# Optimization experiments

Hardware: AMD Instinct MI355X
Metric: run time of the kernel (lower is better)

## Reference

```python
import jax, jax.numpy as jnp
import numpy as np

DIM = 1024
SEQ = 32768
BATCH = 1
MIN_ACTIVE = 0.01
MAX_ACTIVE = 0.1
KMAX = int(MAX_ACTIVE * DIM) + 1  # static upper bound on dynamic k (<= 102)
EPS = 1e-6


def setup_inputs() -> dict:
    key = jax.random.key(0)
    ks = jax.random.split(key, 7)
    h = DIM // 8
    s = 0.02
    return {
        "x": jax.random.normal(ks[0], (BATCH, SEQ, DIM), jnp.float32),
        # complexity_net: Linear(dim, dim//8) -> GELU -> Linear(dim//8, 1) -> Sigmoid
        "w1": jax.random.normal(ks[1], (DIM, h), jnp.float32) * s,
        "b1": jnp.zeros((h,), jnp.float32),
        "w2": jax.random.normal(ks[2], (h, 1), jnp.float32) * s,
        "b2": jnp.zeros((1,), jnp.float32),
        # gate_net: Linear(dim, dim)
        "wg": jax.random.normal(ks[3], (DIM, DIM), jnp.float32) * s,
        "bg": jnp.zeros((DIM,), jnp.float32),
        # running stats (eval mode: used for normalization, not updated)
        "running_mean": jax.random.normal(ks[4], (DIM,), jnp.float32) * 0.1,
        "running_var": jax.random.uniform(ks[5], (DIM,), jnp.float32, minval=0.5, maxval=1.5),
    }


def reference(x, w1, b1, w2, b2, wg, bg, running_mean, running_var):
    # complexity from seq-mean pooled features -> scalar in (0,1)
    pooled = x.mean(axis=1, keepdims=True)                      # (B,1,D)
    hid = jax.nn.gelu(pooled @ w1 + b1, approximate=False)      # torch GELU is exact erf
    complexity = jax.nn.sigmoid(hid @ w2 + b2)                  # (B,1,1)
    active_ratio = MIN_ACTIVE + (MAX_ACTIVE - MIN_ACTIVE) * complexity
    # torch .int() truncates; clamp(min=1). B==1 so k is effectively scalar.
    k = jnp.clip((active_ratio * DIM).astype(jnp.int32), 1, KMAX)  # (B,1,1)

    importance = jnp.abs(x @ wg + bg)                           # (B,S,D)
    importance = (importance - running_mean) / (jnp.sqrt(running_var) + EPS)

    # dynamic-k topk via static-KMAX top_k + threshold at the k-th largest value
    topk_vals, _ = jax.lax.top_k(importance, KMAX)              # (B,S,KMAX)
    idx = jnp.broadcast_to((k - 1).astype(jnp.int32), (x.shape[0], x.shape[1], 1))
    kth = jnp.take_along_axis(topk_vals, idx, axis=-1)          # (B,S,1)
    mask = (importance >= kth).astype(x.dtype)                  # (B,S,D), non-differentiable
    mask = jax.lax.stop_gradient(mask)

    # straight-through combine: forward = x*mask, backward passes grad to all of x
    sparse_x = x * mask + (x - jax.lax.stop_gradient(x)) * (1.0 - mask)

    complexity_mean = complexity.mean()
    active_ratio_mean = active_ratio.mean()
    active_neurons = k.astype(jnp.float32).mean()
    return sparse_x, complexity_mean, active_ratio_mean, active_neurons
```

## Files before the change

kernel.cpp:

```cpp
#include <hip/hip_runtime.h>
#include <cstdint>
#include <cstddef>

#define SEQ 32768
#define DIM 1024
#define HID 128
#define KMAXV 103

using f4 = __attribute__((ext_vector_type(4))) float;
using f2 = __attribute__((ext_vector_type(2))) float;

__global__ __launch_bounds__(256) void pool_partial(const float* __restrict__ x,
                                                    double* __restrict__ part) {
    const int b = blockIdx.x;
    const int t = threadIdx.x;
    const int r0 = b * 128;
    double s0 = 0.0, s1 = 0.0, s2 = 0.0, s3 = 0.0;
    for (int r = 0; r < 128; ++r) {
        const float* row = x + (size_t)(r0 + r) * DIM;
        s0 += (double)row[t];
        s1 += (double)row[t + 256];
        s2 += (double)row[t + 512];
        s3 += (double)row[t + 768];
    }
    double* p = part + (size_t)b * DIM;
    p[t] = s0; p[t + 256] = s1; p[t + 512] = s2; p[t + 768] = s3;
}

__global__ __launch_bounds__(1024) void tiny_net(const double* __restrict__ part,
                                                 const float* __restrict__ w1,
                                                 const float* __restrict__ b1,
                                                 const float* __restrict__ w2,
                                                 const float* __restrict__ b2,
                                                 float* __restrict__ out_scalars,
                                                 int* __restrict__ kout) {
    __shared__ double pooled[DIM];
    __shared__ double hidv[HID];
    const int t = threadIdx.x;

    double s = 0.0;
    for (int b = 0; b < 256; ++b) s += part[(size_t)b * DIM + t];
    pooled[t] = s / (double)SEQ;
    __syncthreads();

    if (t < HID) {
        double h = (double)b1[t];
        for (int d = 0; d < DIM; ++d) h += pooled[d] * (double)w1[d * HID + t];
        h = 0.5 * h * (1.0 + erf(h * 0.70710678118654752440));
        hidv[t] = h;
    }
    __syncthreads();

    if (t == 0) {
        double z = (double)b2[0];
        for (int j = 0; j < HID; ++j) z += hidv[j] * (double)w2[j];
        double c = 1.0 / (1.0 + exp(-z));
        double ar = 0.01 + 0.09 * c;
        int k = (int)(ar * (double)DIM);
        if (k < 1) k = 1;
        if (k > KMAXV) k = KMAXV;
        out_scalars[0] = (float)c;
        out_scalars[1] = (float)ar;
        out_scalars[2] = (float)k;
        *kout = k;
    }
}

#define BM 16
#define CBLOCK 512

template<int K0, int K1, int MODE>
__global__ __launch_bounds__(CBLOCK) void panel_kernel(const float* __restrict__ x,
                                                       const float* __restrict__ wg,
                                                       const float* __restrict__ bg,
                                                       const float* __restrict__ rm,
                                                       const float* __restrict__ rv,
                                                       const int* __restrict__ kptr,
                                                       float* __restrict__ out) {
    __shared__ float lbuf[(MODE == 2) ? 8 * DIM : 1];

    const int t = threadIdx.x;
    const int c2 = t << 1;
    const int row0 = blockIdx.x * BM;

    float pacc[16][2];
#pragma unroll
    for (int m = 0; m < 16; ++m) { pacc[m][0] = 0.0f; pacc[m][1] = 0.0f; }

    const float* wbase = wg + c2;

    f2 wc0 = *(const f2*)(wbase + (size_t)(K0 + 0) * DIM);
    f2 wc1 = *(const f2*)(wbase + (size_t)(K0 + 1) * DIM);
    f2 wc2 = *(const f2*)(wbase + (size_t)(K0 + 2) * DIM);
    f2 wc3 = *(const f2*)(wbase + (size_t)(K0 + 3) * DIM);

    for (int kk0 = K0; kk0 < K1; kk0 += 4) {
        const int kn = (kk0 + 4 < K1) ? (kk0 + 4) : K0;
        const f2 wn0 = *(const f2*)(wbase + (size_t)(kn + 0) * DIM);
        const f2 wn1 = *(const f2*)(wbase + (size_t)(kn + 1) * DIM);
        const f2 wn2 = *(const f2*)(wbase + (size_t)(kn + 2) * DIM);
        const f2 wn3 = *(const f2*)(wbase + (size_t)(kn + 3) * DIM);

        const float* xp = x + (size_t)row0 * DIM + kk0;
#pragma unroll
        for (int m = 0; m < 16; ++m) {
            const f4 xq = *(const f4*)(xp + m * DIM);
            float a0 = pacc[m][0], a1 = pacc[m][1];
            a0 = fmaf(xq[0], wc0[0], a0); a1 = fmaf(xq[0], wc0[1], a1);
            a0 = fmaf(xq[1], wc1[0], a0); a1 = fmaf(xq[1], wc1[1], a1);
            a0 = fmaf(xq[2], wc2[0], a0); a1 = fmaf(xq[2], wc2[1], a1);
            a0 = fmaf(xq[3], wc3[0], a0); a1 = fmaf(xq[3], wc3[1], a1);
            pacc[m][0] = a0; pacc[m][1] = a1;
        }
        wc0 = wn0; wc1 = wn1; wc2 = wn2; wc3 = wn3;
    }

    if constexpr (MODE == 0) {
#pragma unroll
        for (int m = 0; m < 16; ++m) {
            f2 v; v[0] = pacc[m][0]; v[1] = pacc[m][1];
            *(f2*)(out + (size_t)(row0 + m) * DIM + c2) = v;
        }
        return;
    } else if constexpr (MODE == 1) {
#pragma unroll
        for (int m = 0; m < 16; ++m) {
            float* op = out + (size_t)(row0 + m) * DIM + c2;
            f2 d = *(const f2*)op;
            d[0] = d[0] + pacc[m][0];
            d[1] = d[1] + pacc[m][1];
            *(f2*)op = d;
        }
        return;
    } else {
        float dot[16][2];
#pragma unroll
        for (int m = 0; m < 16; ++m) {
            const f2 d = *(const f2*)(out + (size_t)(row0 + m) * DIM + c2);
            dot[m][0] = d[0] + pacc[m][0];
            dot[m][1] = d[1] + pacc[m][1];
        }

        const f2 vbg = *(const f2*)(bg + c2);
        const f2 vrm = *(const f2*)(rm + c2);
        const f2 vrv = *(const f2*)(rv + c2);
        f2 vden;
        vden[0] = sqrtf(vrv[0]) + 1e-6f;
        vden[1] = sqrtf(vrv[1]) + 1e-6f;

        f2 imp[16];
#pragma unroll
        for (int m = 0; m < 16; ++m) {
            imp[m][0] = (fabsf(dot[m][0] + vbg[0]) - vrm[0]) / vden[0];
            imp[m][1] = (fabsf(dot[m][1] + vbg[1]) - vrm[1]) / vden[1];
        }

        int kval = *kptr;
        if (kval < 1) kval = 1;
        if (kval > DIM) kval = DIM;

        float (*selbuf)[DIM] = (float (*)[DIM])lbuf;

        for (int ch = 0; ch < 2; ++ch) {
            __syncthreads();
#pragma unroll
            for (int m = 0; m < 8; ++m)
                *(f2*)(&selbuf[m][c2]) = imp[ch * 8 + m];
            __syncthreads();

            const int w = t >> 6;
            const int l = t & 63;
            const size_t srow = (size_t)(row0 + ch * 8 + w);

            unsigned keys[16];
#pragma unroll
            for (int j = 0; j < 4; ++j) {
                const f4 v = *(const f4*)(&selbuf[w][4 * l + 256 * j]);
#pragma unroll
                for (int i = 0; i < 4; ++i) {
                    const unsigned u = __float_as_uint(v[i]);
                    keys[j * 4 + i] = (u & 0x80000000u) ? ~u : (u | 0x80000000u);
                }
            }

            unsigned pref = 0u;
            for (int b = 31; b >= 0; --b) {
                const unsigned tt = pref | (1u << b);
                int cnt = 0;
#pragma unroll
                for (int j = 0; j < 16; ++j) cnt += (keys[j] >= tt) ? 1 : 0;
#pragma unroll
                for (int off = 32; off >= 1; off >>= 1) cnt += __shfl_xor(cnt, off, 64);
                if (cnt >= kval) pref = tt;
            }

            const float* xr = x + srow * DIM;
            float* orow = out + srow * DIM;
#pragma unroll
            for (int j = 0; j < 4; ++j) {
                const f4 xv = *(const f4*)(xr + 4 * l + 256 * j);
                f4 o;
#pragma unroll
                for (int i = 0; i < 4; ++i) o[i] = (keys[j * 4 + i] >= pref) ? xv[i] : 0.0f;
                *(f4*)(orow + 4 * l + 256 * j) = o;
            }
        }
    }
}

extern "C" void kernel_launch(void* const* d_in, const int* in_sizes, int n_in,
                              void* d_out, int out_size, void* d_ws, size_t ws_size,
                              hipStream_t stream) {
    const float* x  = (const float*)d_in[0];
    const float* w1 = (const float*)d_in[1];
    const float* b1 = (const float*)d_in[2];
    const float* w2 = (const float*)d_in[3];
    const float* b2 = (const float*)d_in[4];
    const float* wg = (const float*)d_in[5];
    const float* bg = (const float*)d_in[6];
    const float* rm = (const float*)d_in[7];
    const float* rv = (const float*)d_in[8];
    float* out = (float*)d_out;

    double* part = (double*)d_ws;
    int* kptr = (int*)((char*)d_ws + (size_t)256 * DIM * sizeof(double));

    pool_partial<<<256, 256, 0, stream>>>(x, part);
    tiny_net<<<1, 1024, 0, stream>>>(part, w1, b1, w2, b2,
                                     out + (size_t)SEQ * DIM, kptr);
    panel_kernel<0,   384,  0><<<SEQ / BM, CBLOCK, 0, stream>>>(x, wg, bg, rm, rv, kptr, out);
    panel_kernel<384, 704,  1><<<SEQ / BM, CBLOCK, 0, stream>>>(x, wg, bg, rm, rv, kptr, out);
    panel_kernel<704, 1024, 2><<<SEQ / BM, CBLOCK, 0, stream>>>(x, wg, bg, rm, rv, kptr, out);
}
```

Baseline: 1.059 ms.

## Fuse second and third K-panels into one kernel and deepen weight prefetch

Merges the second and third K-range panel launches into a single kernel that holds the partial dot products in registers between them. This removes one launch and one full write and read-back of the partial sums through global memory. The weight prefetch is also deepened from one to two stages of four rows. The price is more live registers, which could lower occupancy or cause spills given the already large per-thread accumulator arrays.

Measured after the change: 1.045 ms. Within noise of the previous version (-1.3%).

```diff
diff --git a/kernel.cpp b/kernel.cpp
--- a/kernel.cpp
+++ b/kernel.cpp
@@ -69,37 +69,29 @@
 #define BM 16
 #define CBLOCK 512
 
-template<int K0, int K1, int MODE>
-__global__ __launch_bounds__(CBLOCK) void panel_kernel(const float* __restrict__ x,
-                                                       const float* __restrict__ wg,
-                                                       const float* __restrict__ bg,
-                                                       const float* __restrict__ rm,
-                                                       const float* __restrict__ rv,
-                                                       const int* __restrict__ kptr,
-                                                       float* __restrict__ out) {
-    __shared__ float lbuf[(MODE == 2) ? 8 * DIM : 1];
-
-    const int t = threadIdx.x;
-    const int c2 = t << 1;
-    const int row0 = blockIdx.x * BM;
-
-    float pacc[16][2];
+template<int K0, int K1>
+__device__ __forceinline__ void panel_acc(const float* __restrict__ x,
+                                          const float* __restrict__ wbase,
+                                          int row0, float pacc[16][2]) {
 #pragma unroll
     for (int m = 0; m < 16; ++m) { pacc[m][0] = 0.0f; pacc[m][1] = 0.0f; }
-
-    const float* wbase = wg + c2;
 
     f2 wc0 = *(const f2*)(wbase + (size_t)(K0 + 0) * DIM);
     f2 wc1 = *(const f2*)(wbase + (size_t)(K0 + 1) * DIM);
     f2 wc2 = *(const f2*)(wbase + (size_t)(K0 + 2) * DIM);
     f2 wc3 = *(const f2*)(wbase + (size_t)(K0 + 3) * DIM);
+    f2 wn0 = *(const f2*)(wbase + (size_t)(K0 + 4) * DIM);
+    f2 wn1 = *(const f2*)(wbase + (size_t)(K0 + 5) * DIM);
+    f2 wn2_ = *(const f2*)(wbase + (size_t)(K0 + 6) * DIM);
+    f2 wn3 = *(const f2*)(wbase + (size_t)(K0 + 7) * DIM);
 
     for (int kk0 = K0; kk0 < K1; kk0 += 4) {
-        const int kn = (kk0 + 4 < K1) ? (kk0 + 4) : K0;
-        const f2 wn0 = *(const f2*)(wbase + (size_t)(kn + 0) * DIM);
-        const f2 wn1 = *(const f2*)(wbase + (size_t)(kn + 1) * DIM);
-        const f2 wn2 = *(const f2*)(wbase + (size_t)(kn + 2) * DIM);
-        const f2 wn3 = *(const f2*)(wbase + (size_t)(kn + 3) * DIM);
+        const int kp = kk0 + 8;
+        const int kn2 = (kp < K1) ? kp : K0;
+        const f2 p0 = *(const f2*)(wbase + (size_t)(kn2 + 0) * DIM);
+        const f2 p1 = *(const f2*)(wbase + (size_t)(kn2 + 1) * DIM);
+        const f2 p2 = *(const f2*)(wbase + (size_t)(kn2 + 2) * DIM);
+        const f2 p3 = *(const f2*)(wbase + (size_t)(kn2 + 3) * DIM);
 
         const float* xp = x + (size_t)row0 * DIM + kk0;
 #pragma unroll
@@ -112,98 +104,122 @@
             a0 = fmaf(xq[3], wc3[0], a0); a1 = fmaf(xq[3], wc3[1], a1);
             pacc[m][0] = a0; pacc[m][1] = a1;
         }
-        wc0 = wn0; wc1 = wn1; wc2 = wn2; wc3 = wn3;
-    }
-
-    if constexpr (MODE == 0) {
-#pragma unroll
-        for (int m = 0; m < 16; ++m) {
-            f2 v; v[0] = pacc[m][0]; v[1] = pacc[m][1];
-            *(f2*)(out + (size_t)(row0 + m) * DIM + c2) = v;
-        }
-        return;
-    } else if constexpr (MODE == 1) {
-#pragma unroll
-        for (int m = 0; m < 16; ++m) {
-            float* op = out + (size_t)(row0 + m) * DIM + c2;
-            f2 d = *(const f2*)op;
-            d[0] = d[0] + pacc[m][0];
-            d[1] = d[1] + pacc[m][1];
-            *(f2*)op = d;
-        }
-        return;
-    } else {
-        float dot[16][2];
-#pragma unroll
-        for (int m = 0; m < 16; ++m) {
-            const f2 d = *(const f2*)(out + (size_t)(row0 + m) * DIM + c2);
-            dot[m][0] = d[0] + pacc[m][0];
-            dot[m][1] = d[1] + pacc[m][1];
-        }
-
-        const f2 vbg = *(const f2*)(bg + c2);
-        const f2 vrm = *(const f2*)(rm + c2);
-        const f2 vrv = *(const f2*)(rv + c2);
-        f2 vden;
-        vden[0] = sqrtf(vrv[0]) + 1e-6f;
-        vden[1] = sqrtf(vrv[1]) + 1e-6f;
-
-        f2 imp[16];
-#pragma unroll
-        for (int m = 0; m < 16; ++m) {
-            imp[m][0] = (fabsf(dot[m][0] + vbg[0]) - vrm[0]) / vden[0];
-            imp[m][1] = (fabsf(dot[m][1] + vbg[1]) - vrm[1]) / vden[1];
-        }
-
-        int kval = *kptr;
-        if (kval < 1) kval = 1;
-        if (kval > DIM) kval = DIM;
-
-        float (*selbuf)[DIM] = (float (*)[DIM])lbuf;
-
-        for (int ch = 0; ch < 2; ++ch) {
-            __syncthreads();
-#pragma unroll
-            for (int m = 0; m < 8; ++m)
-                *(f2*)(&selbuf[m][c2]) = imp[ch * 8 + m];
-            __syncthreads();
-
-            const int w = t >> 6;
-            const int l = t & 63;
-            const size_t srow = (size_t)(row0 + ch * 8 + w);
-
-            unsigned keys[16];
-#pragma unroll
-            for (int j = 0; j < 4; ++j) {
-                const f4 v = *(const f4*)(&selbuf[w][4 * l + 256 * j]);
-#pragma unroll
-                for (int i = 0; i < 4; ++i) {
-                    const unsigned u = __float_as_uint(v[i]);
-                    keys[j * 4 + i] = (u & 0x80000000u) ? ~u : (u | 0x80000000u);
-                }
+        wc0 = wn0; wc1 = wn1; wc2 = wn2_; wc3 = wn3;
+        wn0 = p0;  wn1 = p1;  wn2_ = p2;  wn3 = p3;
+    }
+}
+
+__global__ __launch_bounds__(CBLOCK) void panel1_kernel(const float* __restrict__ x,
+                                                        const float* __restrict__ wg,
+                                                        float* __restrict__ out) {
+    const int t = threadIdx.x;
+    const int c2 = t << 1;
+    const int row0 = blockIdx.x * BM;
+
+    float pacc[16][2];
+    panel_acc<0, 384>(x, wg + c2, row0, pacc);
+
+#pragma unroll
+    for (int m = 0; m < 16; ++m) {
+        f2 v; v[0] = pacc[m][0]; v[1] = pacc[m][1];
+        *(f2*)(out + (size_t)(row0 + m) * DIM + c2) = v;
+    }
+}
+
+__global__ __launch_bounds__(CBLOCK) void panel23_kernel(const float* __restrict__ x,
+                                                         const float* __restrict__ wg,
+                                                         const float* __restrict__ bg,
+                                                         const float* __restrict__ rm,
+                                                         const float* __restrict__ rv,
+                                                         const int* __restrict__ kptr,
+                                                         float* __restrict__ out) {
+    __shared__ float lbuf[8 * DIM];
+
+    const int t = threadIdx.x;
+    const int c2 = t << 1;
+    const int row0 = blockIdx.x * BM;
+
+    float pacc[16][2];
+
+    panel_acc<384, 704>(x, wg + c2, row0, pacc);
+    float d12[16][2];
+#pragma unroll
+    for (int m = 0; m < 16; ++m) {
+        const f2 d = *(const f2*)(out + (size_t)(row0 + m) * DIM + c2);
+        d12[m][0] = d[0] + pacc[m][0];
+        d12[m][1] = d[1] + pacc[m][1];
+    }
+
+    panel_acc<704, 1024>(x, wg + c2, row0, pacc);
+    float dot[16][2];
+#pragma unroll
+    for (int m = 0; m < 16; ++m) {
+        dot[m][0] = d12[m][0] + pacc[m][0];
+        dot[m][1] = d12[m][1] + pacc[m][1];
+    }
+
+    const f2 vbg = *(const f2*)(bg + c2);
+    const f2 vrm = *(const f2*)(rm + c2);
+    const f2 vrv = *(const f2*)(rv + c2);
+    f2 vden;
+    vden[0] = sqrtf(vrv[0]) + 1e-6f;
+    vden[1] = sqrtf(vrv[1]) + 1e-6f;
+
+    f2 imp[16];
+#pragma unroll
+    for (int m = 0; m < 16; ++m) {
+        imp[m][0] = (fabsf(dot[m][0] + vbg[0]) - vrm[0]) / vden[0];
+        imp[m][1] = (fabsf(dot[m][1] + vbg[1]) - vrm[1]) / vden[1];
+    }
+
+    int kval = *kptr;
+    if (kval < 1) kval = 1;
+    if (kval > DIM) kval = DIM;
+
+    float (*selbuf)[DIM] = (float (*)[DIM])lbuf;
+
+    for (int ch = 0; ch < 2; ++ch) {
+        __syncthreads();
+#pragma unroll
+        for (int m = 0; m < 8; ++m)
+            *(f2*)(&selbuf[m][c2]) = imp[ch * 8 + m];
+        __syncthreads();
+
+        const int w = t >> 6;
+        const int l = t & 63;
+        const size_t srow = (size_t)(row0 + ch * 8 + w);
+
+        unsigned keys[16];
+#pragma unroll
+        for (int j = 0; j < 4; ++j) {
+            const f4 v = *(const f4*)(&selbuf[w][4 * l + 256 * j]);
+#pragma unroll
+            for (int i = 0; i < 4; ++i) {
+                const unsigned u = __float_as_uint(v[i]);
+                keys[j * 4 + i] = (u & 0x80000000u) ? ~u : (u | 0x80000000u);
             }
-
-            unsigned pref = 0u;
-            for (int b = 31; b >= 0; --b) {
-                const unsigned tt = pref | (1u << b);
-                int cnt = 0;
-#pragma unroll
-                for (int j = 0; j < 16; ++j) cnt += (keys[j] >= tt) ? 1 : 0;
-#pragma unroll
-                for (int off = 32; off >= 1; off >>= 1) cnt += __shfl_xor(cnt, off, 64);
-                if (cnt >= kval) pref = tt;
-            }
-
-            const float* xr = x + srow * DIM;
-            float* orow = out + srow * DIM;
-#pragma unroll
-            for (int j = 0; j < 4; ++j) {
-                const f4 xv = *(const f4*)(xr + 4 * l + 256 * j);
-                f4 o;
-#pragma unroll
-                for (int i = 0; i < 4; ++i) o[i] = (keys[j * 4 + i] >= pref) ? xv[i] : 0.0f;
-                *(f4*)(orow + 4 * l + 256 * j) = o;
-            }
+        }
+
+        unsigned pref = 0u;
+        for (int b = 31; b >= 0; --b) {
+            const unsigned tt = pref | (1u << b);
+            int cnt = 0;
+#pragma unroll
+            for (int j = 0; j < 16; ++j) cnt += (keys[j] >= tt) ? 1 : 0;
+#pragma unroll
+            for (int off = 32; off >= 1; off >>= 1) cnt += __shfl_xor(cnt, off, 64);
+            if (cnt >= kval) pref = tt;
+        }
+
+        const float* xr = x + srow * DIM;
+        float* orow = out + srow * DIM;
+#pragma unroll
+        for (int j = 0; j < 4; ++j) {
+            const f4 xv = *(const f4*)(xr + 4 * l + 256 * j);
+            f4 o;
+#pragma unroll
+            for (int i = 0; i < 4; ++i) o[i] = (keys[j * 4 + i] >= pref) ? xv[i] : 0.0f;
+            *(f4*)(orow + 4 * l + 256 * j) = o;
         }
     }
 }
@@ -228,7 +244,6 @@
     pool_partial<<<256, 256, 0, stream>>>(x, part);
     tiny_net<<<1, 1024, 0, stream>>>(part, w1, b1, w2, b2,
                                      out + (size_t)SEQ * DIM, kptr);
-    panel_kernel<0,   384,  0><<<SEQ / BM, CBLOCK, 0, stream>>>(x, wg, bg, rm, rv, kptr, out);
-    panel_kernel<384, 704,  1><<<SEQ / BM, CBLOCK, 0, stream>>>(x, wg, bg, rm, rv, kptr, out);
-    panel_kernel<704, 1024, 2><<<SEQ / BM, CBLOCK, 0, stream>>>(x, wg, bg, rm, rv, kptr, out);
-}
+    panel1_kernel<<<SEQ / BM, CBLOCK, 0, stream>>>(x, wg, out);
+    panel23_kernel<<<SEQ / BM, CBLOCK, 0, stream>>>(x, wg, bg, rm, rv, kptr, out);
+}
```
